# Performance work log

Measured on AMD Instinct MI355X. Metric: run time of the kernel, lower is better.

Reference implementation:

```python
import jax, jax.numpy as jnp
import numpy as np

HEAD_SIZE = 2000
TAIL_SAMPLE_SIZE = 100
LOGIT_CLIP = 20.0
B, C, K = 2048, 50000, 10
TAIL_SIZE = C - HEAD_SIZE


def psi(u):
    # logistic surrogate: log(1 + exp(-u))
    return jnp.log1p(jnp.exp(-u))


def setup_inputs() -> dict:
    key = jax.random.key(0)
    k1, k2, k3 = jax.random.split(key, 3)
    logits = jax.random.normal(k1, (B, C), dtype=jnp.float32)
    candidates = jax.random.randint(k2, (B, K), 0, C, dtype=jnp.int64)
    sampled_indices = jax.random.randint(k3, (TAIL_SAMPLE_SIZE,), 0, TAIL_SIZE, dtype=jnp.int64)
    return {"logits": logits, "candidates": candidates, "sampled_indices": sampled_indices}


def reference(logits, candidates, sampled_indices):
    logits = jnp.clip(logits, -LOGIT_CLIP, LOGIT_CLIP)
    batch_size, num_classes = logits.shape
    head_size = min(HEAD_SIZE, num_classes)
    tail_size = max(0, num_classes - head_size)

    valid = candidates >= 0                      # [B, K]
    safe_cand = jnp.where(valid, candidates, 0)  # invalid -> col 0, masked below
    rows = jnp.arange(batch_size)[:, None]       # [B, 1] broadcasts over K

    # y_mask[b, c] = 1 if c in candidate set of row b (scatter-max handles dups)
    y_mask = jnp.zeros((batch_size, num_classes), dtype=logits.dtype)
    y_mask = y_mask.at[rows, safe_cand].max(valid.astype(logits.dtype))

    y_counts = y_mask.sum(axis=1)
    y_card = jnp.maximum(y_counts, 1.0)
    avg_candidate_score = (logits * y_mask).sum(axis=1) / y_card
    term1 = psi(avg_candidate_score)

    # head term: penalize non-candidate head logits
    head_logits = logits[:, :head_size]
    head_mask = y_mask[:, :head_size]  # identical to scatter of (valid & cand < head_size)
    term2 = (psi(-head_logits) * (1.0 - head_mask)).sum(axis=1)

    # sampled tail term
    sampled_tail_logits = logits[:, head_size + sampled_indices]  # [B, S]
    # sampled_is_candidate[b, j] = any_k (candidates[b,k] == head_size + sampled_indices[j])
    sampled_is_candidate = jnp.any(
        (candidates[:, :, None] == (head_size + sampled_indices)[None, None, :]) & valid[:, :, None],
        axis=1,
    )  # [B, S] bool
    tail_scale = float(tail_size) / float(sampled_indices.shape[0])
    term3 = (psi(-sampled_tail_logits) * (~sampled_is_candidate).astype(logits.dtype)).sum(axis=1) * tail_scale

    loss = term1 + term2 + term3
    return loss.mean()
```

## Files before the change

### kernel.cpp

```cpp
#include <hip/hip_runtime.h>

#define HEADN   2000
#define NF4     500
#define HALF4   250
#define NSAMP   100
#define KC      10
#define CLIPV   20.0f
#define BATCH   2048
#define NCLASS  50000
#define TAILSCL 480.0f

__device__ __forceinline__ float clipf(float x) {
    return fminf(fmaxf(x, -CLIPV), CLIPV);
}

__device__ __forceinline__ float sp(float x) {
    return __logf(1.0f + __expf(x));
}

__device__ __forceinline__ float sp4(float4 v) {
    return (sp(clipf(v.x)) + sp(clipf(v.y))) + (sp(clipf(v.z)) + sp(clipf(v.w)));
}

__global__ __launch_bounds__(256) void row_loss_wave2(
        const float* __restrict__ logits,
        const int*   __restrict__ cand,
        const int*   __restrict__ samp,
        float*       __restrict__ row_out)
{
    const int tid  = threadIdx.x;
    const int lane = tid & 63;
    const int w    = tid >> 6;
    const int half = w & 1;
    const int row  = blockIdx.x * 2 + (w >> 1);
    const float* lg = logits + (size_t)row * NCLASS;

    const bool sAct = lane < 50;
    const int  scol = HEADN + (sAct ? samp[half * 50 + lane] : 0);
    const float sval = lg[scol];

    const int clm = (lane < KC) ? cand[row * KC + lane] : -1;
    float cval = 0.f;
    if (half == 0 && clm >= 0) cval = lg[clm];

    const int c0 = __shfl(clm, 0), c1 = __shfl(clm, 1), c2 = __shfl(clm, 2),
              c3 = __shfl(clm, 3), c4 = __shfl(clm, 4), c5 = __shfl(clm, 5),
              c6 = __shfl(clm, 6), c7 = __shfl(clm, 7), c8 = __shfl(clm, 8),
              c9 = __shfl(clm, 9);

    const float4* lg4 = (const float4*)lg;
    const int base = half * HALF4;
    const bool t3 = lane < HALF4 - 192;
    float4 v0 = lg4[base + lane];
    float4 v1 = lg4[base + lane + 64];
    float4 v2 = lg4[base + lane + 128];
    float4 v3 = lg4[t3 ? (base + lane + 192) : base];

    float candSum = 0.f, candCnt = 0.f;
    float acc0 = 0.f, acc1 = 0.f;

    acc0 += sp4(v0);
    acc1 += sp4(v1);
    acc0 += sp4(v2);
    if (t3) acc1 += sp4(v3);

    if (sAct) {
        bool isc = (scol == c0) | (scol == c1) | (scol == c2) | (scol == c3) |
                   (scol == c4) | (scol == c5) | (scol == c6) | (scol == c7) |
                   (scol == c8) | (scol == c9);
        if (!isc) acc0 += TAILSCL * sp(clipf(sval));
    }

    if (half == 0 && clm >= 0 && lane < KC) {
        bool distinct = true;
        if (lane > 0 && c0 == clm) distinct = false;
        if (lane > 1 && c1 == clm) distinct = false;
        if (lane > 2 && c2 == clm) distinct = false;
        if (lane > 3 && c3 == clm) distinct = false;
        if (lane > 4 && c4 == clm) distinct = false;
        if (lane > 5 && c5 == clm) distinct = false;
        if (lane > 6 && c6 == clm) distinct = false;
        if (lane > 7 && c7 == clm) distinct = false;
        if (lane > 8 && c8 == clm) distinct = false;
        if (distinct) {
            float x = clipf(cval);
            candSum = x;
            candCnt = 1.f;
            if (clm < HEADN) acc1 -= sp(x);
        }
    }

    float acc = acc0 + acc1;
    #pragma unroll
    for (int off = 32; off > 0; off >>= 1) {
        candSum += __shfl_xor(candSum, off);
        candCnt += __shfl_xor(candCnt, off);
        acc     += __shfl_xor(acc, off);
    }

    __shared__ float sS[4], sC[4], sA[4];
    if (lane == 0) { sS[w] = candSum; sC[w] = candCnt; sA[w] = acc; }
    __syncthreads();
    if (tid == 0) {
        float cs = sS[0] + sS[1], cc = sC[0] + sC[1], a = sA[0] + sA[1];
        float avg = cs / fmaxf(cc, 1.f);
        row_out[row] = sp(-avg) + a;
    }
    if (tid == 128) {
        float cs = sS[2] + sS[3], cc = sC[2] + sC[3], a = sA[2] + sA[3];
        float avg = cs / fmaxf(cc, 1.f);
        row_out[row] = sp(-avg) + a;
    }
}

__global__ __launch_bounds__(64) void mean_kernel(
        const float* __restrict__ row, float* __restrict__ out)
{
    const int lane = threadIdx.x;
    const float4* r4 = (const float4*)row;
    float s = 0.f;
    #pragma unroll
    for (int k = 0; k < BATCH / 4 / 64; ++k) {
        float4 v = r4[lane + 64 * k];
        s += (v.x + v.y) + (v.z + v.w);
    }
    #pragma unroll
    for (int off = 32; off > 0; off >>= 1) s += __shfl_xor(s, off);
    if (lane == 0) out[0] = s / (float)BATCH;
}

extern "C" void kernel_launch(void* const* d_in, const int* in_sizes, int n_in,
                              void* d_out, int out_size, void* d_ws, size_t ws_size,
                              hipStream_t stream) {
    const float* logits = (const float*)d_in[0];
    const int*   cand   = (const int*)d_in[1];
    const int*   samp   = (const int*)d_in[2];
    float* row_out = (float*)d_ws;
    float* out     = (float*)d_out;

    row_loss_wave2<<<BATCH / 2, 256, 0, stream>>>(logits, cand, samp, row_out);
    mean_kernel<<<1, 64, 0, stream>>>(row_out, out);
}
```

Before: 16.14 us.

## Split each row across four waves and defer combination to mean kernel

```diff
diff --git a/kernel.cpp b/kernel.cpp
--- a/kernel.cpp
+++ b/kernel.cpp
@@ -2,7 +2,7 @@
 
 #define HEADN   2000
 #define NF4     500
-#define HALF4   250
+#define QF4     125
 #define NSAMP   100
 #define KC      10
 #define CLIPV   20.0f
@@ -22,26 +22,25 @@
     return (sp(clipf(v.x)) + sp(clipf(v.y))) + (sp(clipf(v.z)) + sp(clipf(v.w)));
 }
 
-__global__ __launch_bounds__(256) void row_loss_wave2(
+__global__ __launch_bounds__(256) void row_loss_q(
         const float* __restrict__ logits,
         const int*   __restrict__ cand,
         const int*   __restrict__ samp,
-        float*       __restrict__ row_out)
+        float*       __restrict__ partial)
 {
     const int tid  = threadIdx.x;
     const int lane = tid & 63;
     const int w    = tid >> 6;
-    const int half = w & 1;
-    const int row  = blockIdx.x * 2 + (w >> 1);
+    const int row  = blockIdx.x;
     const float* lg = logits + (size_t)row * NCLASS;
 
-    const bool sAct = lane < 50;
-    const int  scol = HEADN + (sAct ? samp[half * 50 + lane] : 0);
+    const bool  sAct = lane < (NSAMP / 4);
+    const int   scol = HEADN + (sAct ? samp[w * (NSAMP / 4) + lane] : 0);
     const float sval = lg[scol];
 
     const int clm = (lane < KC) ? cand[row * KC + lane] : -1;
     float cval = 0.f;
-    if (half == 0 && clm >= 0) cval = lg[clm];
+    if (w == 0 && clm >= 0) cval = lg[clm];
 
     const int c0 = __shfl(clm, 0), c1 = __shfl(clm, 1), c2 = __shfl(clm, 2),
               c3 = __shfl(clm, 3), c4 = __shfl(clm, 4), c5 = __shfl(clm, 5),
@@ -49,20 +48,13 @@
               c9 = __shfl(clm, 9);
 
     const float4* lg4 = (const float4*)lg;
-    const int base = half * HALF4;
-    const bool t3 = lane < HALF4 - 192;
-    float4 v0 = lg4[base + lane];
-    float4 v1 = lg4[base + lane + 64];
-    float4 v2 = lg4[base + lane + 128];
-    float4 v3 = lg4[t3 ? (base + lane + 192) : base];
+    const int  base = w * QF4;
+    const bool t1   = lane < QF4 - 64;
+    const float4 v0 = lg4[base + lane];
+    const float4 v1 = lg4[t1 ? (base + 64 + lane) : base];
 
-    float candSum = 0.f, candCnt = 0.f;
-    float acc0 = 0.f, acc1 = 0.f;
-
-    acc0 += sp4(v0);
-    acc1 += sp4(v1);
-    acc0 += sp4(v2);
-    if (t3) acc1 += sp4(v3);
+    float acc0 = sp4(v0);
+    float acc1 = t1 ? sp4(v1) : 0.f;
 
     if (sAct) {
         bool isc = (scol == c0) | (scol == c1) | (scol == c2) | (scol == c3) |
@@ -71,7 +63,8 @@
         if (!isc) acc0 += TAILSCL * sp(clipf(sval));
     }
 
-    if (half == 0 && clm >= 0 && lane < KC) {
+    float candSum = 0.f, candCnt = 0.f;
+    if (w == 0 && clm >= 0 && lane < KC) {
         bool distinct = true;
         if (lane > 0 && c0 == clm) distinct = false;
         if (lane > 1 && c1 == clm) distinct = false;
@@ -93,40 +86,37 @@
     float acc = acc0 + acc1;
     #pragma unroll
     for (int off = 32; off > 0; off >>= 1) {
+        acc     += __shfl_xor(acc, off);
         candSum += __shfl_xor(candSum, off);
         candCnt += __shfl_xor(candCnt, off);
-        acc     += __shfl_xor(acc, off);
     }
 
-    __shared__ float sS[4], sC[4], sA[4];
-    if (lane == 0) { sS[w] = candSum; sC[w] = candCnt; sA[w] = acc; }
-    __syncthreads();
-    if (tid == 0) {
-        float cs = sS[0] + sS[1], cc = sC[0] + sC[1], a = sA[0] + sA[1];
-        float avg = cs / fmaxf(cc, 1.f);
-        row_out[row] = sp(-avg) + a;
-    }
-    if (tid == 128) {
-        float cs = sS[2] + sS[3], cc = sC[2] + sC[3], a = sA[2] + sA[3];
-        float avg = cs / fmaxf(cc, 1.f);
-        row_out[row] = sp(-avg) + a;
+    if (lane == 0) {
+        if (w == 0) {
+            float avg = candSum / fmaxf(candCnt, 1.f);
+            acc += sp(-avg);
+        }
+        partial[row * 4 + w] = acc;
     }
 }
 
-__global__ __launch_bounds__(64) void mean_kernel(
-        const float* __restrict__ row, float* __restrict__ out)
+__global__ __launch_bounds__(256) void mean_kernel(
+        const float* __restrict__ part, float* __restrict__ out)
 {
-    const int lane = threadIdx.x;
-    const float4* r4 = (const float4*)row;
+    const int tid = threadIdx.x;
+    const float4* p4 = (const float4*)part;
     float s = 0.f;
     #pragma unroll
-    for (int k = 0; k < BATCH / 4 / 64; ++k) {
-        float4 v = r4[lane + 64 * k];
+    for (int k = 0; k < (BATCH * 4) / 4 / 256; ++k) {
+        float4 v = p4[tid + 256 * k];
         s += (v.x + v.y) + (v.z + v.w);
     }
     #pragma unroll
     for (int off = 32; off > 0; off >>= 1) s += __shfl_xor(s, off);
-    if (lane == 0) out[0] = s / (float)BATCH;
+    __shared__ float sw[4];
+    if ((tid & 63) == 0) sw[tid >> 6] = s;
+    __syncthreads();
+    if (tid == 0) out[0] = (sw[0] + sw[1] + sw[2] + sw[3]) / (float)BATCH;
 }
 
 extern "C" void kernel_launch(void* const* d_in, const int* in_sizes, int n_in,
@@ -135,9 +125,9 @@
     const float* logits = (const float*)d_in[0];
     const int*   cand   = (const int*)d_in[1];
     const int*   samp   = (const int*)d_in[2];
-    float* row_out = (float*)d_ws;
+    float* partial = (float*)d_ws;
     float* out     = (float*)d_out;
 
-    row_loss_wave2<<<BATCH / 2, 256, 0, stream>>>(logits, cand, samp, row_out);
-    mean_kernel<<<1, 64, 0, stream>>>(row_out, out);
+    row_loss_q<<<BATCH, 256, 0, stream>>>(logits, cand, samp, partial);
+    mean_kernel<<<1, 256, 0, stream>>>(partial, out);
 }
```

New measurement: 16.02 us. About the same (-0.8%).
